# Optimization experiments

Measured on AMD Instinct MI355X. Metric: run time of the kernel, lower is better.

The kernel has to match this reference:

```python
import jax, jax.numpy as jnp
import numpy as np

DPH, NH = 64, 4           # dim_per_head, num_head -> dim_total = 256
ALPHA_CONV = 0.1          # LeakyReLU alpha in DarknetConv2D_BN_Leaky
ALPHA_DENSE = 0.3         # Keras LeakyReLU default alpha (Dense activation)


def _leaky(x, a):
    return jnp.where(x > 0, x, a * x)


def _cbl(x, W, g, b):
    """1x1 conv (no bias) + inference BatchNorm (folded affine) + LeakyReLU(0.1)."""
    y = jnp.einsum('nwhc,cd->nwhd', x, W)
    return _leaky(y * g + b, ALPHA_CONV)


def setup_inputs() -> dict:
    key = jax.random.key(0)
    ks = jax.random.split(key, 26)
    N, Wg, Hg, C = 16, 64, 64, 256
    D = DPH * NH

    def n(k, shape, s=1.0):
        return jax.random.normal(k, shape, jnp.float32) * s

    return {
        'inputs': n(ks[0], (N, Wg, Hg, C)),
        'style':  n(ks[1], (N, C)),
        'W_dense': n(ks[2], (C, C), 0.05),
        'Wq_c': n(ks[3], (C, D), 0.05), 'gq_c': 1.0 + n(ks[4], (D,), 0.02), 'bq_c': n(ks[5], (D,), 0.02),
        'Wk_c': n(ks[6], (C, D), 0.05), 'gk_c': 1.0 + n(ks[7], (D,), 0.02), 'bk_c': n(ks[8], (D,), 0.02),
        'Wv_c': n(ks[9], (C, D), 0.05), 'gv_c': 1.0 + n(ks[10], (D,), 0.02), 'bv_c': n(ks[11], (D,), 0.02),
        'Wq_p': n(ks[12], (C, D), 0.05), 'gq_p': 1.0 + n(ks[13], (D,), 0.02), 'bq_p': n(ks[14], (D,), 0.02),
        'Wk_p': n(ks[15], (C, D), 0.05), 'gk_p': 1.0 + n(ks[16], (D,), 0.02), 'bk_p': n(ks[17], (D,), 0.02),
        'Wv_p': n(ks[18], (C, D), 0.05), 'gv_p': 1.0 + n(ks[19], (D,), 0.02), 'bv_p': n(ks[20], (D,), 0.02),
        'W_ch':  n(ks[21], (2 * D, D), 0.02),
        'W_pos': n(ks[22], (2 * D, NH), 0.02),
        'W_out': n(ks[23], (2 * D, C), 0.05),
        'g_out': 1.0 + n(ks[24], (C,), 0.02),
        'b_out': n(ks[25], (C,), 0.02),
    }


def reference(inputs, style, W_dense,
              Wq_c, gq_c, bq_c, Wk_c, gk_c, bk_c, Wv_c, gv_c, bv_c,
              Wq_p, gq_p, bq_p, Wk_p, gk_p, bk_p, Wv_p, gv_p, bv_p,
              W_ch, W_pos, W_out, g_out, b_out):
    N, Wg, Hg, C = inputs.shape
    D = DPH * NH
    scale = 1.0 / jnp.sqrt(jnp.float32(DPH))

    # style -> query feature, [N,1,1,C]
    q0 = _leaky(style @ W_dense, ALPHA_DENSE)[:, None, None, :]

    # ---------- channel-wise attention branch ----------
    qc = _cbl(q0, Wq_c, gq_c, bq_c)          # [N,1,1,D]
    kc = _cbl(inputs, Wk_c, gk_c, bk_c)      # [N,W,H,D]
    vc = _cbl(inputs, Wv_c, gv_c, bv_c)      # [N,W,H,D]
    catc = jnp.concatenate([jnp.broadcast_to(qc, kc.shape), kc], axis=-1)  # [N,W,H,2D]
    # einsum('awhd,awhdc->ac') with w broadcast over a,w,h == plain contraction
    a_c = jnp.einsum('nwhd,dc->nc', catc, W_ch) * scale                     # [N,D]
    a_c = jax.nn.softmax(a_c.reshape(N, DPH, NH), axis=1).reshape(N, 1, 1, D)
    o_ch = a_c * vc                                                          # [N,W,H,D]

    # ---------- position-wise attention branch ----------
    qp = _cbl(q0, Wq_p, gq_p, bq_p)
    kp = _cbl(inputs, Wk_p, gk_p, bk_p)
    vp = _cbl(inputs, Wv_p, gv_p, bv_p)
    catp = jnp.concatenate([jnp.broadcast_to(qp, kp.shape), kp], axis=-1)   # [N,W,H,2D]
    a_p = jnp.einsum('nwhd,dm->nwhm', catp, W_pos) * scale                  # [N,W,H,NH]
    a_p = jax.nn.softmax(a_p.reshape(N, Wg * Hg, NH), axis=1)
    a_p = a_p.reshape(N, Wg, Hg, NH, 1)
    o_pos = (a_p * vp.reshape(N, Wg, Hg, NH, DPH)).reshape(N, Wg, Hg, D)

    # ---------- fuse + output 1x1 conv ----------
    out = _cbl(jnp.concatenate([o_ch, o_pos], axis=-1), W_out, g_out, b_out)  # [N,W,H,C]
    return out
```

## Files before the change

### kernel.cpp

```cpp
#include <hip/hip_runtime.h>
#include <hip/hip_bf16.h>

#define PTOT  65536
#define SCALE 0.125f

typedef __attribute__((ext_vector_type(8))) short short8;
typedef __attribute__((ext_vector_type(4))) float f32x4;

__device__ __forceinline__ float leaky(float x, float a) { return x > 0.f ? x : a * x; }

__device__ __forceinline__ unsigned short f2bfbits(float f) {
    __hip_bfloat16 h = __float2bfloat16(f); unsigned short u;
    __builtin_memcpy(&u, &h, 2); return u;
}

__device__ __forceinline__ void gld16(const void* g, void* l) {
    __builtin_amdgcn_global_load_lds(
        (const __attribute__((address_space(1))) unsigned int*)g,
        (__attribute__((address_space(3))) unsigned int*)l, 16, 0, 0);
}

__device__ __forceinline__ void mfma_step64(const char* Aseg, const char* Bs,
                                            int l, int wm, int wn, f32x4 acc[2][4])
{
#pragma unroll
    for (int ks = 0; ks < 2; ++ks) {
        short8 af[2], bfr[4];
        const int c = ks * 4 + (l >> 4);
        const int sw = ((c ^ (l & 7)) << 4);
#pragma unroll
        for (int mf = 0; mf < 2; ++mf)
            af[mf] = *(const short8*)(Aseg + (wm * 32 + mf * 16 + (l & 15)) * 128 + sw);
#pragma unroll
        for (int nf = 0; nf < 4; ++nf)
            bfr[nf] = *(const short8*)(Bs + (wn * 64 + nf * 16 + (l & 15)) * 128 + sw);
#pragma unroll
        for (int mf = 0; mf < 2; ++mf)
#pragma unroll
            for (int nf = 0; nf < 4; ++nf)
                acc[mf][nf] = __builtin_amdgcn_mfma_f32_16x16x32_bf16(af[mf], bfr[nf], acc[mf][nf], 0, 0, 0);
    }
}

__device__ __forceinline__ void stageB(const __hip_bfloat16* Bt, int ldk, int k0,
                                       char* Bs, int w, int l, int cg)
{
#pragma unroll
    for (int pass = 0; pass < 4; ++pass) {
        const int col = w * 8 + (l >> 3) + pass * 64;
        gld16(Bt + (size_t)col * ldk + k0 + cg * 8, Bs + (w * 8 + pass * 64) * 128);
    }
}

__device__ __forceinline__ void stageA64(const __hip_bfloat16* Abf, int pix0, int k0,
                                         char* dst, int w, int l, int cg)
{
    const int row = w * 8 + (l >> 3);
    gld16(Abf + (size_t)(pix0 + row) * 256 + k0 + cg * 8, dst + w * 8 * 128);
}

template<int MODE>
__device__ __forceinline__ void k1_body(int bb, int t,
    const float* __restrict__ vin, const float* __restrict__ W,
    const float* __restrict__ g, const float* __restrict__ bv,
    float* __restrict__ vout, float* s0, float (*pr)[32])
{
    const int n = bb >> 3, c0 = (bb & 7) * 32;
    if (t < 256) s0[t] = vin[n * 256 + t];
    __syncthreads();
    const int kp = t >> 5, ci = t & 31, c = c0 + ci;
    float a = 0.f;
#pragma unroll 8
    for (int i = 0; i < 32; ++i) {
        const int k = kp * 32 + i;
        a += s0[k] * W[k * 256 + c];
    }
    pr[kp][ci] = a;
    __syncthreads();
    if (t < 32) {
        float s = 0.f;
#pragma unroll
        for (int q = 0; q < 8; ++q) s += pr[q][t];
        const int cc = c0 + t;
        if constexpr (MODE == 0)      vout[n * 256 + cc] = leaky(s, 0.3f);
        else if constexpr (MODE == 1) vout[n * 256 + cc] = leaky(s * g[cc] + bv[cc], 0.1f);
        else                          vout[n * 256 + cc] = 4096.f * s;
    }
}

template<int MODE>
__global__ __launch_bounds__(256) void k1g(
    const float* __restrict__ vin, const float* __restrict__ W,
    const float* __restrict__ g, const float* __restrict__ bv,
    float* __restrict__ vout)
{
    __shared__ float s0[256];
    __shared__ float pr[8][32];
    k1_body<MODE>(blockIdx.x, threadIdx.x, vin, W, g, bv, vout, s0, pr);
}

__global__ __launch_bounds__(256) void kW_cvt(
    const float* __restrict__ W0, const float* __restrict__ W1,
    const float* __restrict__ W2, const float* __restrict__ W3,
    const float* __restrict__ Wout,
    __hip_bfloat16* __restrict__ WT4, __hip_bfloat16* __restrict__ WoutT,
    const float* __restrict__ style, const float* __restrict__ W_dense,
    float* __restrict__ s1ws)
{
    __shared__ float s0[256];
    __shared__ float pr[8][32];
    const int b = blockIdx.x, t = threadIdx.x;
    if (b < 1024) {
        const int w = b >> 8, c = b & 255;
        const float* W = (w == 0) ? W0 : (w == 1) ? W1 : (w == 2) ? W2 : W3;
        WT4[((size_t)w * 256 + c) * 256 + t] = __float2bfloat16(W[t * 256 + c]);
    } else if (b < 1280) {
        const int c = b - 1024;
        WoutT[(size_t)c * 512 + t]       = __float2bfloat16(Wout[t * 256 + c]);
        WoutT[(size_t)c * 512 + t + 256] = __float2bfloat16(Wout[(t + 256) * 256 + c]);
    } else {
        k1_body<0>(b - 1280, t, style, W_dense, nullptr, nullptr, s1ws, s0, pr);
    }
}

__global__ __launch_bounds__(512, 4) void kA(
    const float* __restrict__ in, __hip_bfloat16* __restrict__ in_bf,
    const __hip_bfloat16* __restrict__ BkcT, const __hip_bfloat16* __restrict__ BkpT,
    const float* __restrict__ gkc, const float* __restrict__ bkc,
    const float* __restrict__ gkp, const float* __restrict__ bkp,
    const float* __restrict__ W_pos,
    float* __restrict__ partial, float* __restrict__ logits)
{
    __shared__ alignas(16) char smem[73728];
    char* Afull = smem;
    char* Bs    = smem + 32768;
    float* wpos_s = (float*)(smem + 65536);
    float* red    = (float*)(smem + 69632);
    float* sc     = (float*)(smem + 69632);

    const int t = threadIdx.x, l = t & 63, w = t >> 6;
    const int wm = w >> 2, wn = w & 3;
    const int pix0 = blockIdx.x * 64;
    const int cg = (l & 7) ^ ((l >> 3) & 7);

    for (int e = t; e < 1024; e += 512) wpos_s[e] = W_pos[1024 + e];

    {
        const int row = t >> 3, c = t & 7;
#pragma unroll
        for (int seg = 0; seg < 4; ++seg) {
            const float* p = in + (size_t)(pix0 + row) * 256 + seg * 64 + c * 8;
            const float4 x0 = *(const float4*)p, x1 = *(const float4*)(p + 4);
            short8 v;
            v[0]=(short)f2bfbits(x0.x); v[1]=(short)f2bfbits(x0.y); v[2]=(short)f2bfbits(x0.z); v[3]=(short)f2bfbits(x0.w);
            v[4]=(short)f2bfbits(x1.x); v[5]=(short)f2bfbits(x1.y); v[6]=(short)f2bfbits(x1.z); v[7]=(short)f2bfbits(x1.w);
            *(short8*)(Afull + seg * 8192 + row * 128 + ((c ^ (row & 7)) << 4)) = v;
            *(short8*)(in_bf + (size_t)(pix0 + row) * 256 + seg * 64 + c * 8) = v;
        }
    }

    f32x4 acc[2][4];
#pragma unroll
    for (int i = 0; i < 2; ++i)
#pragma unroll
        for (int j = 0; j < 4; ++j) acc[i][j] = (f32x4)0.f;
    for (int s = 0; s < 4; ++s) {
        __syncthreads();
        stageB(BkcT, 256, s * 64, Bs, w, l, cg);
        __syncthreads();
        mfma_step64(Afull + s * 8192, Bs, l, wm, wn, acc);
    }
#pragma unroll
    for (int nf = 0; nf < 4; ++nf) {
        const int col = wn * 64 + nf * 16 + (l & 15);
        const float g = gkc[col], bb = bkc[col];
        float cs = 0.f;
#pragma unroll
        for (int mf = 0; mf < 2; ++mf)
#pragma unroll
            for (int r = 0; r < 4; ++r) cs += leaky(acc[mf][nf][r] * g + bb, 0.1f);
        cs += __shfl_xor(cs, 16);
        cs += __shfl_xor(cs, 32);
        if (l < 16) red[wm * 256 + wn * 64 + nf * 16 + l] = cs;
    }
    __syncthreads();
    if (t < 256) partial[(size_t)blockIdx.x * 256 + t] = red[t] + red[256 + t];

#pragma unroll
    for (int i = 0; i < 2; ++i)
#pragma unroll
        for (int j = 0; j < 4; ++j) acc[i][j] = (f32x4)0.f;
    for (int s = 0; s < 4; ++s) {
        __syncthreads();
        stageB(BkpT, 256, s * 64, Bs, w, l, cg);
        __syncthreads();
        mfma_step64(Afull + s * 8192, Bs, l, wm, wn, acc);
    }
    __syncthreads();
#pragma unroll
    for (int mf = 0; mf < 2; ++mf)
#pragma unroll
        for (int r = 0; r < 4; ++r) {
            const int row_l = wm * 32 + mf * 16 + (l >> 4) * 4 + r;
            float pm0 = 0.f, pm1 = 0.f, pm2 = 0.f, pm3 = 0.f;
#pragma unroll
            for (int nf = 0; nf < 4; ++nf) {
                const int col = wn * 64 + nf * 16 + (l & 15);
                const float g = gkp[col], bb = bkp[col];
                const float v = leaky(acc[mf][nf][r] * g + bb, 0.1f);
                pm0 += v * wpos_s[col * 4 + 0];
                pm1 += v * wpos_s[col * 4 + 1];
                pm2 += v * wpos_s[col * 4 + 2];
                pm3 += v * wpos_s[col * 4 + 3];
            }
#pragma unroll
            for (int mask = 1; mask <= 8; mask <<= 1) {
                pm0 += __shfl_xor(pm0, mask);
                pm1 += __shfl_xor(pm1, mask);
                pm2 += __shfl_xor(pm2, mask);
                pm3 += __shfl_xor(pm3, mask);
            }
            if ((l & 15) == 0) {
                float* sp = &sc[row_l * 16 + wn];
                sp[0] = pm0; sp[4] = pm1; sp[8] = pm2; sp[12] = pm3;
            }
        }
    __syncthreads();
    if (t < 256) {
        const int row = t >> 2, m = t & 3;
        const float sum = sc[row * 16 + m * 4 + 0] + sc[row * 16 + m * 4 + 1]
                        + sc[row * 16 + m * 4 + 2] + sc[row * 16 + m * 4 + 3];
        logits[(size_t)(pix0 + row) * 4 + m] = SCALE * sum;
    }
}

__global__ __launch_bounds__(256) void k2bc(
    const float* __restrict__ partial,
    const float* __restrict__ acq, const float* __restrict__ W_ch,
    float* __restrict__ a_c, float* __restrict__ lg)
{
    const int t = threadIdx.x;
    if (blockIdx.x < 16) {
        __shared__ float ks[256], lgs[256];
        const int n = blockIdx.x;
        float s = 0.f;
        for (int tt = 0; tt < 64; ++tt) s += partial[(size_t)(n * 64 + tt) * 256 + t];
        ks[t] = s;
        __syncthreads();
        float bot = 0.f;
        for (int d = 0; d < 256; ++d) bot += ks[d] * W_ch[(256 + d) * 256 + t];
        const float L = SCALE * (acq[n * 256 + t] + bot);
        lgs[t] = L;
        __syncthreads();
        const int nh = t & 3;
        float mx = -1e30f;
        for (int i = 0; i < 64; ++i) mx = fmaxf(mx, lgs[i * 4 + nh]);
        float sum = 0.f;
        for (int i = 0; i < 64; ++i) sum += __expf(lgs[i * 4 + nh] - mx);
        a_c[n * 256 + t] = __expf(L - mx) / sum;
    } else {
        __shared__ float r[256];
        const int bb = blockIdx.x - 16;
        const int n = bb >> 2, m = bb & 3;
        const int base = n * 4096;
        float v[16];
        float mx = -1e30f;
#pragma unroll
        for (int i = 0; i < 16; ++i) {
            v[i] = lg[(size_t)(base + i * 256 + t) * 4 + m];
            mx = fmaxf(mx, v[i]);
        }
        r[t] = mx; __syncthreads();
        for (int s = 128; s > 0; s >>= 1) { if (t < s) r[t] = fmaxf(r[t], r[t + s]); __syncthreads(); }
        mx = r[0]; __syncthreads();
        float sum = 0.f;
#pragma unroll
        for (int i = 0; i < 16; ++i) { v[i] = __expf(v[i] - mx); sum += v[i]; }
        r[t] = sum; __syncthreads();
        for (int s = 128; s > 0; s >>= 1) { if (t < s) r[t] += r[t + s]; __syncthreads(); }
        const float rinv = 1.f / r[0];
#pragma unroll
        for (int i = 0; i < 16; ++i) lg[(size_t)(base + i * 256 + t) * 4 + m] = v[i] * rinv;
    }
}

__global__ __launch_bounds__(512, 4) void kB(
    const __hip_bfloat16* __restrict__ Abf,
    const __hip_bfloat16* __restrict__ BvcT, const __hip_bfloat16* __restrict__ BvpT,
    const __hip_bfloat16* __restrict__ WoutT,
    const float* __restrict__ gvc, const float* __restrict__ bvc,
    const float* __restrict__ gvp, const float* __restrict__ bvp,
    const float* __restrict__ a_c, const float* __restrict__ apos,
    const float* __restrict__ g_out, const float* __restrict__ b_out,
    float* __restrict__ outp)
{
    __shared__ alignas(16) char smem[75776];
    char* As   = smem;
    char* Bs   = smem + 8192;
    char* A2   = smem + 40960;
    float* ac_s = (float*)(smem + 73728);
    float* ap_s = (float*)(smem + 74752);

    const int t = threadIdx.x, l = t & 63, w = t >> 6;
    const int wm = w >> 2, wn = w & 3;
    const int pix0 = blockIdx.x * 64;
    const int n = pix0 >> 12;
    const int cg = (l & 7) ^ ((l >> 3) & 7);

    if (t < 256) {
        ac_s[t] = a_c[n * 256 + t];
        ap_s[t] = apos[(size_t)pix0 * 4 + t];
    }

    f32x4 acc2[2][4];
#pragma unroll
    for (int i = 0; i < 2; ++i)
#pragma unroll
        for (int j = 0; j < 4; ++j) acc2[i][j] = (f32x4)0.f;

    for (int half = 0; half < 2; ++half) {
        const __hip_bfloat16* Bv = half ? BvpT : BvcT;
        const float* gv = half ? gvp : gvc;
        const float* bv = half ? bvp : bvc;

        f32x4 acc1[2][4];
#pragma unroll
        for (int i = 0; i < 2; ++i)
#pragma unroll
            for (int j = 0; j < 4; ++j) acc1[i][j] = (f32x4)0.f;
        for (int s = 0; s < 4; ++s) {
            __syncthreads();
            stageA64(Abf, pix0, s * 64, As, w, l, cg);
            stageB(Bv, 256, s * 64, Bs, w, l, cg);
            __syncthreads();
            mfma_step64(As, Bs, l, wm, wn, acc1);
        }
        __syncthreads();
#pragma unroll
        for (int nf = 0; nf < 4; ++nf) {
            const int col = wn * 64 + nf * 16 + (l & 15);
            const float g = gv[col], bb = bv[col];
            const int c2 = (col & 63) >> 3, cb = (col & 7) * 2;
            const float sc_c = ac_s[col];
#pragma unroll
            for (int mf = 0; mf < 2; ++mf)
#pragma unroll
                for (int r = 0; r < 4; ++r) {
                    const int row = wm * 32 + mf * 16 + (l >> 4) * 4 + r;
                    float v = leaky(acc1[mf][nf][r] * g + bb, 0.1f);
                    v *= half ? ap_s[row * 4 + wn] : sc_c;
                    *(unsigned short*)(A2 + wn * 8192 + row * 128
                                       + ((c2 ^ (row & 7)) << 4) + cb) = f2bfbits(v);
                }
        }
        for (int s = 0; s < 4; ++s) {
            __syncthreads();
            stageB(WoutT, 512, half * 256 + s * 64, Bs, w, l, cg);
            __syncthreads();
            mfma_step64(A2 + s * 8192, Bs, l, wm, wn, acc2);
        }
    }

#pragma unroll
    for (int nf = 0; nf < 4; ++nf) {
        const int col = wn * 64 + nf * 16 + (l & 15);
        const float g = g_out[col], bb = b_out[col];
#pragma unroll
        for (int mf = 0; mf < 2; ++mf)
#pragma unroll
            for (int r = 0; r < 4; ++r) {
                const int p = pix0 + wm * 32 + mf * 16 + (l >> 4) * 4 + r;
                outp[(size_t)p * 256 + col] = leaky(acc2[mf][nf][r] * g + bb, 0.1f);
            }
    }
}

extern "C" void kernel_launch(void* const* d_in, const int* in_sizes, int n_in,
                              void* d_out, int out_size, void* d_ws, size_t ws_size,
                              hipStream_t stream)
{
    const float* inputs  = (const float*)d_in[0];
    const float* style   = (const float*)d_in[1];
    const float* W_dense = (const float*)d_in[2];
    const float* Wq_c = (const float*)d_in[3];
    const float* gq_c = (const float*)d_in[4];
    const float* bq_c = (const float*)d_in[5];
    const float* Wk_c = (const float*)d_in[6];
    const float* gk_c = (const float*)d_in[7];
    const float* bk_c = (const float*)d_in[8];
    const float* Wv_c = (const float*)d_in[9];
    const float* gv_c = (const float*)d_in[10];
    const float* bv_c = (const float*)d_in[11];
    const float* Wk_p = (const float*)d_in[15];
    const float* gk_p = (const float*)d_in[16];
    const float* bk_p = (const float*)d_in[17];
    const float* Wv_p = (const float*)d_in[18];
    const float* gv_p = (const float*)d_in[19];
    const float* bv_p = (const float*)d_in[20];
    const float* W_ch  = (const float*)d_in[21];
    const float* W_pos = (const float*)d_in[22];
    const float* W_out = (const float*)d_in[23];
    const float* g_out = (const float*)d_in[24];
    const float* b_out = (const float*)d_in[25];

    float* ws = (float*)d_ws;
    float* s1ws    = ws;
    float* qcws    = ws + 4096;
    float* acq     = ws + 8192;
    float* a_c     = ws + 12288;
    float* partial = ws + 16384;
    float* logits  = ws + 278528;
    __hip_bfloat16* in_bf = (__hip_bfloat16*)(ws + 540672);
    __hip_bfloat16* WT4   = (__hip_bfloat16*)(ws + 8929280);
    __hip_bfloat16* WoutT = (__hip_bfloat16*)(ws + 9060352);

    kW_cvt<<<1408, 256, 0, stream>>>(Wk_c, Wv_c, Wk_p, Wv_p, W_out,
                                     WT4, WoutT, style, W_dense, s1ws);
    k1g<1><<<128, 256, 0, stream>>>(s1ws, Wq_c, gq_c, bq_c, qcws);
    k1g<2><<<128, 256, 0, stream>>>(qcws, W_ch, nullptr, nullptr, acq);

    kA<<<1024, 512, 0, stream>>>(inputs, in_bf, WT4, WT4 + 2 * 65536,
                                 gk_c, bk_c, gk_p, bk_p, W_pos, partial, logits);

    k2bc<<<80, 256, 0, stream>>>(partial, acq, W_ch, a_c, logits);

    kB<<<1024, 512, 0, stream>>>(in_bf, WT4 + 65536, WT4 + 3 * 65536, WoutT,
                                 gv_c, bv_c, gv_p, bv_p, a_c, logits,
                                 g_out, b_out, (float*)d_out);
}
```

Baseline: 143.6 us.

## Merge Kc/Kp GEMMs into one 512-wide pass and share A staging in V GEMMs

```diff
diff --git a/kernel.cpp b/kernel.cpp
--- a/kernel.cpp
+++ b/kernel.cpp
@@ -135,13 +135,10 @@
     char* Afull = smem;
     char* Bs    = smem + 32768;
     float* wpos_s = (float*)(smem + 65536);
-    float* red    = (float*)(smem + 69632);
     float* sc     = (float*)(smem + 69632);
 
     const int t = threadIdx.x, l = t & 63, w = t >> 6;
-    const int wm = w >> 2, wn = w & 3;
     const int pix0 = blockIdx.x * 64;
-    const int cg = (l & 7) ^ ((l >> 3) & 7);
 
     for (int e = t; e < 1024; e += 512) wpos_s[e] = W_pos[1024 + e];
 
@@ -159,72 +156,92 @@
         }
     }
 
-    f32x4 acc[2][4];
-#pragma unroll
-    for (int i = 0; i < 2; ++i)
+    f32x4 acc[4][4];
+#pragma unroll
+    for (int i = 0; i < 4; ++i)
 #pragma unroll
         for (int j = 0; j < 4; ++j) acc[i][j] = (f32x4)0.f;
-    for (int s = 0; s < 4; ++s) {
-        __syncthreads();
-        stageB(BkcT, 256, s * 64, Bs, w, l, cg);
-        __syncthreads();
-        mfma_step64(Afull + s * 8192, Bs, l, wm, wn, acc);
-    }
-#pragma unroll
-    for (int nf = 0; nf < 4; ++nf) {
-        const int col = wn * 64 + nf * 16 + (l & 15);
-        const float g = gkc[col], bb = bkc[col];
-        float cs = 0.f;
-#pragma unroll
-        for (int mf = 0; mf < 2; ++mf)
-#pragma unroll
-            for (int r = 0; r < 4; ++r) cs += leaky(acc[mf][nf][r] * g + bb, 0.1f);
-        cs += __shfl_xor(cs, 16);
-        cs += __shfl_xor(cs, 32);
-        if (l < 16) red[wm * 256 + wn * 64 + nf * 16 + l] = cs;
-    }
-    __syncthreads();
-    if (t < 256) partial[(size_t)blockIdx.x * 256 + t] = red[t] + red[256 + t];
-
-#pragma unroll
-    for (int i = 0; i < 2; ++i)
-#pragma unroll
-        for (int j = 0; j < 4; ++j) acc[i][j] = (f32x4)0.f;
-    for (int s = 0; s < 4; ++s) {
-        __syncthreads();
-        stageB(BkpT, 256, s * 64, Bs, w, l, cg);
-        __syncthreads();
-        mfma_step64(Afull + s * 8192, Bs, l, wm, wn, acc);
-    }
-    __syncthreads();
-#pragma unroll
-    for (int mf = 0; mf < 2; ++mf)
-#pragma unroll
-        for (int r = 0; r < 4; ++r) {
-            const int row_l = wm * 32 + mf * 16 + (l >> 4) * 4 + r;
-            float pm0 = 0.f, pm1 = 0.f, pm2 = 0.f, pm3 = 0.f;
+
+    for (int s = 0; s < 8; ++s) {
+        __syncthreads();
+        {
+            const int cg = (l & 3) ^ ((l >> 3) & 3);
+#pragma unroll
+            for (int p = 0; p < 4; ++p) {
+                const int col = w * 16 + (l >> 2) + p * 128;
+                const __hip_bfloat16* src = (p < 2)
+                    ? BkcT + (size_t)col * 256
+                    : BkpT + (size_t)(col - 256) * 256;
+                gld16(src + s * 32 + cg * 8, Bs + (size_t)(w * 16 + p * 128) * 64);
+            }
+        }
+        __syncthreads();
+        {
+            const int c8 = (s & 1) * 4 + (l >> 4);
+            const char* Aseg = Afull + (s >> 1) * 8192;
+            short8 af[4], bfr[4];
+#pragma unroll
+            for (int mf = 0; mf < 4; ++mf) {
+                const int row = mf * 16 + (l & 15);
+                af[mf] = *(const short8*)(Aseg + row * 128 + ((c8 ^ (row & 7)) << 4));
+            }
 #pragma unroll
             for (int nf = 0; nf < 4; ++nf) {
-                const int col = wn * 64 + nf * 16 + (l & 15);
-                const float g = gkp[col], bb = bkp[col];
-                const float v = leaky(acc[mf][nf][r] * g + bb, 0.1f);
-                pm0 += v * wpos_s[col * 4 + 0];
-                pm1 += v * wpos_s[col * 4 + 1];
-                pm2 += v * wpos_s[col * 4 + 2];
-                pm3 += v * wpos_s[col * 4 + 3];
-            }
-#pragma unroll
-            for (int mask = 1; mask <= 8; mask <<= 1) {
-                pm0 += __shfl_xor(pm0, mask);
-                pm1 += __shfl_xor(pm1, mask);
-                pm2 += __shfl_xor(pm2, mask);
-                pm3 += __shfl_xor(pm3, mask);
-            }
-            if ((l & 15) == 0) {
-                float* sp = &sc[row_l * 16 + wn];
-                sp[0] = pm0; sp[4] = pm1; sp[8] = pm2; sp[12] = pm3;
-            }
-        }
+                const int brow = w * 64 + nf * 16 + (l & 15);
+                bfr[nf] = *(const short8*)(Bs + brow * 64 + (((l >> 4) ^ ((brow >> 1) & 3)) << 4));
+            }
+#pragma unroll
+            for (int mf = 0; mf < 4; ++mf)
+#pragma unroll
+                for (int nf = 0; nf < 4; ++nf)
+                    acc[mf][nf] = __builtin_amdgcn_mfma_f32_16x16x32_bf16(af[mf], bfr[nf], acc[mf][nf], 0, 0, 0);
+        }
+    }
+
+    if (w < 4) {
+#pragma unroll
+        for (int nf = 0; nf < 4; ++nf) {
+            const int col = w * 64 + nf * 16 + (l & 15);
+            const float g = gkc[col], bb = bkc[col];
+            float cs = 0.f;
+#pragma unroll
+            for (int mf = 0; mf < 4; ++mf)
+#pragma unroll
+                for (int r = 0; r < 4; ++r) cs += leaky(acc[mf][nf][r] * g + bb, 0.1f);
+            cs += __shfl_xor(cs, 16);
+            cs += __shfl_xor(cs, 32);
+            if (l < 16) partial[(size_t)blockIdx.x * 256 + col] = cs;
+        }
+    } else {
+#pragma unroll
+        for (int mf = 0; mf < 4; ++mf)
+#pragma unroll
+            for (int r = 0; r < 4; ++r) {
+                const int row = mf * 16 + (l >> 4) * 4 + r;
+                float pm0 = 0.f, pm1 = 0.f, pm2 = 0.f, pm3 = 0.f;
+#pragma unroll
+                for (int nf = 0; nf < 4; ++nf) {
+                    const int kcol = (w - 4) * 64 + nf * 16 + (l & 15);
+                    const float g = gkp[kcol], bb = bkp[kcol];
+                    const float v = leaky(acc[mf][nf][r] * g + bb, 0.1f);
+                    pm0 += v * wpos_s[kcol * 4 + 0];
+                    pm1 += v * wpos_s[kcol * 4 + 1];
+                    pm2 += v * wpos_s[kcol * 4 + 2];
+                    pm3 += v * wpos_s[kcol * 4 + 3];
+                }
+#pragma unroll
+                for (int mask = 1; mask <= 8; mask <<= 1) {
+                    pm0 += __shfl_xor(pm0, mask);
+                    pm1 += __shfl_xor(pm1, mask);
+                    pm2 += __shfl_xor(pm2, mask);
+                    pm3 += __shfl_xor(pm3, mask);
+                }
+                if ((l & 15) == 0) {
+                    float* sp = &sc[row * 16 + (w - 4)];
+                    sp[0] = pm0; sp[4] = pm1; sp[8] = pm2; sp[12] = pm3;
+                }
+            }
+    }
     __syncthreads();
     if (t < 256) {
         const int row = t >> 2, m = t & 3;
@@ -312,53 +329,71 @@
         ap_s[t] = apos[(size_t)pix0 * 4 + t];
     }
 
-    f32x4 acc2[2][4];
+    f32x4 acc1c[2][4], acc1p[2][4], acc2[2][4];
 #pragma unroll
     for (int i = 0; i < 2; ++i)
 #pragma unroll
-        for (int j = 0; j < 4; ++j) acc2[i][j] = (f32x4)0.f;
-
-    for (int half = 0; half < 2; ++half) {
-        const __hip_bfloat16* Bv = half ? BvpT : BvcT;
-        const float* gv = half ? gvp : gvc;
-        const float* bv = half ? bvp : bvc;
-
-        f32x4 acc1[2][4];
-#pragma unroll
-        for (int i = 0; i < 2; ++i)
-#pragma unroll
-            for (int j = 0; j < 4; ++j) acc1[i][j] = (f32x4)0.f;
-        for (int s = 0; s < 4; ++s) {
-            __syncthreads();
-            stageA64(Abf, pix0, s * 64, As, w, l, cg);
-            stageB(Bv, 256, s * 64, Bs, w, l, cg);
-            __syncthreads();
-            mfma_step64(As, Bs, l, wm, wn, acc1);
-        }
-        __syncthreads();
-#pragma unroll
-        for (int nf = 0; nf < 4; ++nf) {
-            const int col = wn * 64 + nf * 16 + (l & 15);
-            const float g = gv[col], bb = bv[col];
-            const int c2 = (col & 63) >> 3, cb = (col & 7) * 2;
-            const float sc_c = ac_s[col];
-#pragma unroll
-            for (int mf = 0; mf < 2; ++mf)
-#pragma unroll
-                for (int r = 0; r < 4; ++r) {
-                    const int row = wm * 32 + mf * 16 + (l >> 4) * 4 + r;
-                    float v = leaky(acc1[mf][nf][r] * g + bb, 0.1f);
-                    v *= half ? ap_s[row * 4 + wn] : sc_c;
-                    *(unsigned short*)(A2 + wn * 8192 + row * 128
-                                       + ((c2 ^ (row & 7)) << 4) + cb) = f2bfbits(v);
-                }
-        }
-        for (int s = 0; s < 4; ++s) {
-            __syncthreads();
-            stageB(WoutT, 512, half * 256 + s * 64, Bs, w, l, cg);
-            __syncthreads();
-            mfma_step64(A2 + s * 8192, Bs, l, wm, wn, acc2);
-        }
+        for (int j = 0; j < 4; ++j) {
+            acc1c[i][j] = (f32x4)0.f;
+            acc1p[i][j] = (f32x4)0.f;
+            acc2[i][j]  = (f32x4)0.f;
+        }
+
+    for (int s = 0; s < 4; ++s) {
+        __syncthreads();
+        stageA64(Abf, pix0, s * 64, As, w, l, cg);
+        stageB(BvcT, 256, s * 64, Bs, w, l, cg);
+        __syncthreads();
+        mfma_step64(As, Bs, l, wm, wn, acc1c);
+        __syncthreads();
+        stageB(BvpT, 256, s * 64, Bs, w, l, cg);
+        __syncthreads();
+        mfma_step64(As, Bs, l, wm, wn, acc1p);
+    }
+
+#pragma unroll
+    for (int nf = 0; nf < 4; ++nf) {
+        const int col = wn * 64 + nf * 16 + (l & 15);
+        const float g = gvc[col], bb = bvc[col];
+        const int c2 = (col & 63) >> 3, cb = (col & 7) * 2;
+        const float sc_c = ac_s[col];
+#pragma unroll
+        for (int mf = 0; mf < 2; ++mf)
+#pragma unroll
+            for (int r = 0; r < 4; ++r) {
+                const int row = wm * 32 + mf * 16 + (l >> 4) * 4 + r;
+                float v = leaky(acc1c[mf][nf][r] * g + bb, 0.1f) * sc_c;
+                *(unsigned short*)(A2 + wn * 8192 + row * 128
+                                   + ((c2 ^ (row & 7)) << 4) + cb) = f2bfbits(v);
+            }
+    }
+    for (int s = 0; s < 4; ++s) {
+        __syncthreads();
+        stageB(WoutT, 512, s * 64, Bs, w, l, cg);
+        __syncthreads();
+        mfma_step64(A2 + s * 8192, Bs, l, wm, wn, acc2);
+    }
+    __syncthreads();
+#pragma unroll
+    for (int nf = 0; nf < 4; ++nf) {
+        const int col = wn * 64 + nf * 16 + (l & 15);
+        const float g = gvp[col], bb = bvp[col];
+        const int c2 = (col & 63) >> 3, cb = (col & 7) * 2;
+#pragma unroll
+        for (int mf = 0; mf < 2; ++mf)
+#pragma unroll
+            for (int r = 0; r < 4; ++r) {
+                const int row = wm * 32 + mf * 16 + (l >> 4) * 4 + r;
+                float v = leaky(acc1p[mf][nf][r] * g + bb, 0.1f) * ap_s[row * 4 + wn];
+                *(unsigned short*)(A2 + wn * 8192 + row * 128
+                                   + ((c2 ^ (row & 7)) << 4) + cb) = f2bfbits(v);
+            }
+    }
+    for (int s = 0; s < 4; ++s) {
+        __syncthreads();
+        stageB(WoutT, 512, 256 + s * 64, Bs, w, l, cg);
+        __syncthreads();
+        mfma_step64(A2 + s * 8192, Bs, l, wm, wn, acc2);
     }
 
 #pragma unroll
```

After: 134.5 us (median of 4 runs). -6.3%, faster.
